# Optimization experiments

Measured on AMD Instinct MI355X. Metric: run time of the kernel, lower is better.

## Reference

```python
import jax, jax.numpy as jnp
import numpy as np

# QMon (monDEQ, Winston & Kolter): conv pre-net -> MONSingleConv + MONBorderReLU solved
# with Peaceman-Rachford splitting -> border crop -> MLP head.
BATCH = 256
C = 64            # DEQ channels
N = 9             # DEQ spatial dim (in_dim=9)
K = 3             # MONSingleConv kernel size
M_STRONG = 0.1    # m (strong monotonicity)
ALPHA = 1.0
TOL = 1e-5
MAX_ITER = 50
OUT_FEATURES = 18


def conv2d(x, w, b=None, stride=1):
    y = jax.lax.conv_general_dilated(x, w, (stride, stride), 'VALID',
                                     dimension_numbers=('NCHW', 'OIHW', 'NCHW'))
    if b is not None:
        y = y + b[None, :, None, None]
    return y


def circ_conv(x, w, b=None):
    # circular-padded 'same' conv (cpad + valid conv in the torch code)
    p = (w.shape[2] - 1) // 2
    xp = jnp.pad(x, ((0, 0), (0, 0), (p, p), (p, p)), mode='wrap')
    return conv2d(xp, w, b)


def circ_conv_T(x, w):
    # adjoint of circular conv = circular conv with spatially-flipped, channel-transposed kernel
    wt = jnp.transpose(jnp.flip(w, (2, 3)), (1, 0, 2, 3))
    return circ_conv(x, wt)


def W_multiply(z, A_w, g):
    # W z = (1-m) z - g * A^T A z, with A Frobenius-normalized
    An = A_w / jnp.linalg.norm(A_w)
    Az = circ_conv(z, An)
    ATAz = circ_conv_T(Az, An)
    return (1.0 - M_STRONG) * z - g * ATAz


def build_inverse(A_w, g, n):
    # ((1+alpha) I - alpha W)^{-1} per 2D-DFT frequency (circular conv is block-circulant)
    An = A_w / jnp.linalg.norm(A_w)
    co, ci, k, _ = An.shape
    p = (k - 1) // 2
    kimg = jnp.zeros((co, ci, n, n), An.dtype)
    for dx in range(k):
        for dy in range(k):
            kimg = kimg.at[:, :, (dx - p) % n, (dy - p) % n].set(An[:, :, dx, dy])
    Af = jnp.conj(jnp.fft.fft2(kimg)).transpose(2, 3, 0, 1)  # (n,n,O,I): A_hat(w)
    I = jnp.eye(co, dtype=Af.dtype)
    c = (1.0 + ALPHA) - ALPHA * (1.0 - M_STRONG)
    Mmat = c * I + (ALPHA * g).astype(Af.dtype) * jnp.einsum('xyoi,xyoj->xyij', jnp.conj(Af), Af)
    return jnp.linalg.inv(Mmat)  # (n,n,C,C) complex


def apply_inverse(Vinv, z):
    zf = jnp.fft.fft2(z)                                  # (B,C,n,n)
    yf = jnp.einsum('xyoc,bcxy->boxy', Vinv, zf)
    return jnp.real(jnp.fft.ifft2(yf)).astype(z.dtype)


def mon_deq(xpre, U_w, U_b, A_w, g):
    n = xpre.shape[-1]
    bias = circ_conv(xpre, U_w, U_b)
    Vinv = build_inverse(A_w, g, n)
    mask = jnp.pad(jnp.ones((n - 2, n - 2), xpre.dtype), 1)[None, None]  # MONBorderReLU border=1
    brelu = lambda v: jax.nn.relu(v) * mask
    z0 = jnp.zeros_like(bias)

    def body(state):
        z, u, err, it = state
        u12 = 2.0 * z - u
        z12 = apply_inverse(Vinv, u12 + ALPHA * bias)
        un = 2.0 * z12 - u12
        zn = brelu(un)
        err = jnp.linalg.norm(zn - z) / (1e-6 + jnp.linalg.norm(zn))
        return zn, un, err, it + 1

    def cond(state):
        _, _, err, it = state
        return (err > TOL) & (it < MAX_ITER)

    z, u, err, it = jax.lax.while_loop(cond, body, (z0, z0, jnp.asarray(1.0, xpre.dtype), 0))
    # final pass with the linear operator (as in the torch forward after the no_grad solve)
    return brelu(W_multiply(z, A_w, g) + bias)


def setup_inputs() -> dict:
    key = jax.random.key(0)
    ks = jax.random.split(key, 12)

    def u(k, shape, fan_in):
        b = 1.0 / np.sqrt(fan_in)
        return jax.random.uniform(k, shape, jnp.float32, -b, b)

    x = jax.random.uniform(ks[0], (BATCH, 4, 84, 84), jnp.float32) * 255.0
    return dict(
        x=x,
        conv1_w=u(ks[1], (32, 4, 8, 8), 4 * 8 * 8), conv1_b=u(ks[2], (32,), 4 * 8 * 8),
        conv2_w=u(ks[3], (64, 32, 4, 4), 32 * 4 * 4), conv2_b=u(ks[4], (64,), 32 * 4 * 4),
        U_w=u(ks[5], (C, C, K, K), C * K * K), U_b=u(ks[6], (C,), C * K * K),
        A_w=u(ks[7], (C, C, K, K), C * K * K), g=jnp.asarray(1.0, jnp.float32),
        fc1_w=u(ks[8], (512, 3136), 3136), fc1_b=u(ks[9], (512,), 3136),
        fc2_w=u(ks[10], (OUT_FEATURES, 512), 512), fc2_b=u(ks[11], (OUT_FEATURES,), 512),
    )


def reference(x, conv1_w, conv1_b, conv2_w, conv2_b, U_w, U_b, A_w, g,
              fc1_w, fc1_b, fc2_w, fc2_b):
    h = jax.nn.relu(conv2d(x / 255.0, conv1_w, conv1_b, stride=4))   # (B,32,20,20)
    h = jax.nn.relu(conv2d(h, conv2_w, conv2_b, stride=2))           # (B,64,9,9)
    z = mon_deq(h, U_w, U_b, A_w, g)                                 # (B,64,9,9)
    z = z[:, :, 1:-1, 1:-1].reshape(z.shape[0], -1)                  # (B,3136)
    h = jax.nn.relu(z @ fc1_w.T + fc1_b)
    return h @ fc2_w.T + fc2_b
```

## Files before the change

### kernel.cpp

```cpp
#include <hip/hip_runtime.h>


#define NB 256
#define NCH 64
#define NP 81
#define NIMG (NB*NCH)
#define MAXIT 50
#define NCAN 41
#define CANON(l) ((l) < 5 ? (l) : (l) + 4)

constexpr float C9[9] = {
  1.0f, 0.76604444311897803f, 0.17364817766693041f, -0.5f,
  -0.93969262078590843f, -0.93969262078590843f, -0.5f,
  0.17364817766693041f, 0.76604444311897803f };
constexpr float S9[9] = {
  0.0f, 0.64278760968653936f, 0.98480775301220802f, 0.86602540378443871f,
  0.34202014332566877f, -0.34202014332566877f, -0.86602540378443871f,
  -0.98480775301220802f, -0.64278760968653936f };

__constant__ float COS9[9] = {
  1.0f, 0.76604444311897803f, 0.17364817766693041f, -0.5f,
  -0.93969262078590843f, -0.93969262078590843f, -0.5f,
  0.17364817766693041f, 0.76604444311897803f };
__constant__ float SIN9[9] = {
  0.0f, 0.64278760968653936f, 0.98480775301220802f, 0.86602540378443871f,
  0.34202014332566877f, -0.34202014332566877f, -0.86602540378443871f,
  -0.98480775301220802f, -0.64278760968653936f };

__global__ __launch_bounds__(256) void k_norm(const float* __restrict__ Aw,
                                              float* __restrict__ sc) {
    __shared__ float red[256];
    float s = 0.f;
    for (int i = threadIdx.x; i < 64*64*9; i += 256) { float a = Aw[i]; s += a*a; }
    red[threadIdx.x] = s; __syncthreads();
    for (int w = 128; w > 0; w >>= 1) {
        if (threadIdx.x < w) red[threadIdx.x] += red[threadIdx.x + w];
        __syncthreads();
    }
    if (threadIdx.x == 0) { float n = sqrtf(red[0]); sc[0] = n; sc[1] = 1.f/n; }
}

__global__ __launch_bounds__(512, 4) void k_conv1(const float* __restrict__ x,
                                                  const float* __restrict__ w,
                                                  const float* __restrict__ bb,
                                                  float* __restrict__ y) {
    __shared__ float xl[2*7056];
    int blk = blockIdx.x, tid = threadIdx.x;
    int b = blk >> 1, og = (blk & 1) << 4;
    float acc[16];
    #pragma unroll
    for (int o = 0; o < 16; ++o) acc[o] = 0.f;
    int p = tid, oy = p/20, ox = p%20;
    for (int cp = 0; cp < 2; ++cp) {
        __syncthreads();
        const float4* xg = (const float4*)(x + b*28224 + cp*14112);
        for (int i = tid; i < 3528; i += 512) ((float4*)xl)[i] = xg[i];
        __syncthreads();
        if (p < 400) {
            #pragma unroll
            for (int ci = 0; ci < 2; ++ci)
            #pragma unroll
            for (int ky = 0; ky < 8; ++ky) {
                const float* xr = xl + ci*7056 + (oy*4+ky)*84 + ox*4;
                float4 x0 = *(const float4*)xr;
                float4 x1 = *(const float4*)(xr+4);
                const float* wr = w + og*256 + (cp*2+ci)*64 + ky*8;
                #pragma unroll
                for (int o = 0; o < 16; ++o) {
                    const float* wo = wr + o*256;
                    acc[o] += x0.x*wo[0] + x0.y*wo[1] + x0.z*wo[2] + x0.w*wo[3]
                            + x1.x*wo[4] + x1.y*wo[5] + x1.z*wo[6] + x1.w*wo[7];
                }
            }
        }
    }
    if (p < 400) {
        #pragma unroll
        for (int o = 0; o < 16; ++o)
            y[b*12800 + (og+o)*400 + p] = fmaxf(acc[o]*(1.f/255.f) + bb[og+o], 0.f);
    }
}

__global__ __launch_bounds__(512, 4) void k_conv2(const float* __restrict__ h1,
                                                  const float* __restrict__ w2,
                                                  const float* __restrict__ b2,
                                                  float* __restrict__ h2) {
    int blk = blockIdx.x, tid = threadIdx.x;
    int b = blk >> 1, og = (blk & 1) << 5;
    __shared__ float hl[12800];
    for (int i = tid; i < 12800; i += 512) {
        int ci = i / 400, pix = i % 400, iy = pix / 20, ix = pix % 20;
        hl[ci*400 + ((iy&1)*2 + (ix&1))*100 + (iy>>1)*10 + (ix>>1)] = h1[b*12800 + i];
    }
    __syncthreads();
    for (int idx = tid; idx < 2592; idx += 512) {
        int o = og + idx/81, p = idx%81, oy = p/9, ox = p%9;
        float acc = 0.f;
        const float* wo = w2 + o*512;
        for (int ci = 0; ci < 32; ci++) {
            const float* base = hl + ci*400;
            const float* wb = wo + ci*16;
            #pragma unroll
            for (int ky = 0; ky < 4; ky++)
            #pragma unroll
            for (int kx = 0; kx < 4; kx++)
                acc += base[((ky&1)*2 + (kx&1))*100 + (oy + (ky>>1))*10 + (ox + (kx>>1))]
                     * wb[ky*4 + kx];
        }
        h2[b*5184 + o*81 + p] = fmaxf(acc + b2[o], 0.f);
    }
}

__global__ __launch_bounds__(512, 4) void k_bias(const float* __restrict__ h2,
                                                 const float* __restrict__ Uw,
                                                 const float* __restrict__ Ub,
                                                 float* __restrict__ biasT) {
    int blk = blockIdx.x, tid = threadIdx.x;
    int b = blk >> 1, og = (blk & 1) << 5;
    __shared__ float h2l[5184];
    __shared__ float bt[2592];
    for (int i = tid; i < 5184; i += 512) h2l[i] = h2[b*5184 + i];
    __syncthreads();
    for (int idx = tid; idx < 2592; idx += 512) {
        int oc = idx/81, o = og + oc, p = idx%81, i0 = p/9, j0 = p%9;
        int im = (i0+8)%9, ip = (i0+1)%9, jm = (j0+8)%9, jp = (j0+1)%9;
        int r0 = im*9, r1 = i0*9, r2 = ip*9;
        float acc = 0.f;
        const float* wo = Uw + o*576;
        for (int ci = 0; ci < 64; ci++) {
            const float* hb = h2l + ci*81;
            const float* wb = wo + ci*9;
            acc += hb[r0+jm]*wb[0] + hb[r0+j0]*wb[1] + hb[r0+jp]*wb[2]
                 + hb[r1+jm]*wb[3] + hb[r1+j0]*wb[4] + hb[r1+jp]*wb[5]
                 + hb[r2+jm]*wb[6] + hb[r2+j0]*wb[7] + hb[r2+jp]*wb[8];
        }
        bt[oc*81 + p] = acc + Ub[o];
    }
    __syncthreads();
    for (int idx = tid; idx < 2592; idx += 512) {
        int p = idx >> 5, o32 = idx & 31;
        biasT[p*NIMG + b*64 + og + o32] = bt[o32*81 + p];
    }
}

__global__ __launch_bounds__(256) void k_af(const float* __restrict__ Aw,
                                            const float* __restrict__ sc,
                                            float2* __restrict__ Af) {
    int l = blockIdx.x; int f = CANON(l);
    int x = f/9, y = f%9;
    float inv = sc[1];
    for (int pr = threadIdx.x; pr < 4096; pr += 256) {
        const float* a = Aw + pr*9;
        float re = 0.f, im = 0.f;
        #pragma unroll
        for (int dx = 0; dx < 3; dx++)
        #pragma unroll
        for (int dy = 0; dy < 3; dy++) {
            int tt = (x*(dx+8) + y*(dy+8)) % 9;
            float v = a[dx*3+dy] * inv;
            re += v * COS9[tt]; im += v * SIN9[tt];
        }
        Af[f*4096 + pr] = make_float2(re, im);
    }
}

__global__ __launch_bounds__(256) void k_mw(const float2* __restrict__ Af,
                                            const float* __restrict__ gp,
                                            float2* __restrict__ Mmat,
                                            float2* __restrict__ WmT) {
    int l = blockIdx.x >> 2, q = blockIdx.x & 3;
    int f = CANON(l);
    float g = gp[0];
    __shared__ float2 Al[4096];
    for (int i = threadIdx.x; i < 4096; i += 256) Al[i] = Af[f*4096 + i];
    __syncthreads();
    int e = q*1024 + threadIdx.x;
    #pragma unroll
    for (int rep = 0; rep < 4; ++rep, e += 256) {
        int i = e >> 6, j = e & 63;
        float sr = 0.f, si = 0.f;
        for (int o = 0; o < 64; o++) {
            float2 a = Al[o*64 + i], b = Al[o*64 + j];
            sr += a.x*b.x + a.y*b.y;
            si += a.x*b.y - a.y*b.x;
        }
        Mmat[f*4096 + e] = make_float2((i==j ? 1.1f : 0.f) + g*sr, g*si);
        WmT [f*4096 + j*64 + i] = make_float2((i==j ? 0.9f : 0.f) - g*sr, -g*si);
    }
}

__global__ __launch_bounds__(256) void k_inv(float2* __restrict__ Mio) {
    int f = CANON((int)blockIdx.x);
    __shared__ float2 Mt[64*65];
    __shared__ float2 rowk[2][64];
    __shared__ float2 fcol[2][64];
    int tid = threadIdx.x;
    int i = tid & 63, jg = tid >> 6;
    float2* Mg = Mio + f*4096;
    for (int e = tid; e < 4096; e += 256) Mt[(e>>6)*65 + (e&63)] = Mg[e];
    __syncthreads();
    float2 r[16];
    #pragma unroll
    for (int jj = 0; jj < 16; ++jj) r[jj] = Mt[i*65 + jg*16 + jj];

    for (int k = 0; k < 64; ++k) {
        int buf = k & 1;
        if (i == k) {
            #pragma unroll
            for (int jj = 0; jj < 16; ++jj) rowk[buf][jg*16 + jj] = r[jj];
        }
        if (jg == (k >> 4)) {
            int sel = k & 15;
            float2 v = r[0];
            #pragma unroll
            for (int jj = 1; jj < 16; ++jj) v = (sel == jj) ? r[jj] : v;
            fcol[buf][i] = v;
        }
        __syncthreads();
        float2 d = rowk[buf][k];
        float den = 1.f / (d.x*d.x + d.y*d.y);
        float pr = d.x*den, pi = -d.y*den;
        float2 fi = fcol[buf][i];
        bool piv = (i == k);
        #pragma unroll
        for (int jj = 0; jj < 16; ++jj) {
            int j = jg*16 + jj;
            float2 rw = rowk[buf][j];
            float2 rkj = (j == k) ? make_float2(pr, pi)
                                  : make_float2(rw.x*pr - rw.y*pi,
                                                rw.x*pi + rw.y*pr);
            if (piv) {
                r[jj] = rkj;
            } else {
                float bx = (j == k) ? 0.f : r[jj].x;
                float by = (j == k) ? 0.f : r[jj].y;
                r[jj] = make_float2(bx - (fi.x*rkj.x - fi.y*rkj.y),
                                    by - (fi.x*rkj.y + fi.y*rkj.x));
            }
        }
    }
    __syncthreads();
    #pragma unroll
    for (int jj = 0; jj < 16; ++jj) Mt[(jg*16 + jj)*65 + i] = r[jj];
    __syncthreads();
    for (int e = tid; e < 4096; e += 256) Mg[e] = Mt[(e>>6)*65 + (e&63)];
}

__global__ __launch_bounds__(576) void k_fft(const float* __restrict__ biasT,
                                             float2* __restrict__ Tf) {
    __shared__ float2 T1[81*64];
    int lane = threadIdx.x & 63, j = threadIdx.x >> 6;
    int gimg = blockIdx.x*64 + lane;
    {
        int r = j;
        float tn[9];
        #pragma unroll
        for (int xc = 0; xc < 9; ++xc) tn[xc] = biasT[(r*9 + xc)*NIMG + gimg];
        #pragma unroll
        for (int ky = 0; ky < 9; ++ky) {
            float sr = 0.f, si = 0.f;
            #pragma unroll
            for (int xx = 0; xx < 9; ++xx) {
                const int m = (ky*xx) % 9;
                sr += tn[xx]*C9[m];
                si -= tn[xx]*S9[m];
            }
            T1[(r*9 + ky)*64 + lane] = make_float2(sr, si);
        }
    }
    __syncthreads();
    {
        int ky = j;
        float2 s[9];
        #pragma unroll
        for (int r = 0; r < 9; ++r) s[r] = T1[(r*9 + ky)*64 + lane];
        #pragma unroll
        for (int kx = 0; kx < 5; ++kx) {
            float fr = 0.f, fi = 0.f;
            #pragma unroll
            for (int r = 0; r < 9; ++r) {
                const int m = (kx*r) % 9;
                fr += s[r].x*C9[m] + s[r].y*S9[m];
                fi += s[r].y*C9[m] - s[r].x*S9[m];
            }
            if (kx > 0 || ky < 5)
                Tf[(kx*9 + ky)*NIMG + gimg] = make_float2(fr, fi);
        }
    }
}

__global__ __launch_bounds__(256) void k_mv(const float2* __restrict__ Tf,
                                            float2* __restrict__ Yf,
                                            const float2* __restrict__ V) {
    int l = blockIdx.x >> 4, bc = blockIdx.x & 15;
    int f = CANON(l);
    int lane = threadIdx.x & 63;
    int wid  = __builtin_amdgcn_readfirstlane((int)(threadIdx.x >> 6));
    int b0 = bc*16 + wid*4;
    const float2* Vg = V + f*4096 + lane;
    const float2* Tg = Tf + f*NIMG + b0*64;
    float2 a0 = make_float2(0.f,0.f), a1 = a0, a2 = a0, a3 = a0;
    #pragma unroll 8
    for (int c = 0; c < 64; ++c) {
        float2 v = Vg[c*64];
        float2 t0 = Tg[c], t1 = Tg[64+c], t2 = Tg[128+c], t3 = Tg[192+c];
        a0.x += v.x*t0.x - v.y*t0.y; a0.y += v.x*t0.y + v.y*t0.x;
        a1.x += v.x*t1.x - v.y*t1.y; a1.y += v.x*t1.y + v.y*t1.x;
        a2.x += v.x*t2.x - v.y*t2.y; a2.y += v.x*t2.y + v.y*t2.x;
        a3.x += v.x*t3.x - v.y*t3.y; a3.y += v.x*t3.y + v.y*t3.x;
    }
    float2* Yg = Yf + f*NIMG + b0*64 + lane;
    Yg[0] = a0; Yg[64] = a1; Yg[128] = a2; Yg[192] = a3;
}

__global__ __launch_bounds__(576) void k_fuse(const float2* __restrict__ Yf,
                                              float* __restrict__ u12T,
                                              const float* __restrict__ biasT,
                                              float2* __restrict__ Tf,
                                              int last) {
    __shared__ float2 T1[81*64];
    int lane = threadIdx.x & 63, j = threadIdx.x >> 6;
    int gimg = blockIdx.x*64 + lane;
    {
        int ky = j;
        float2 y[9];
        #pragma unroll
        for (int kx = 0; kx < 9; ++kx) {
            int fc; bool cj;
            if (kx == 0)      { cj = (ky >= 5); fc = cj ? (9 - ky) : ky; }
            else if (kx <= 4) { cj = false;     fc = kx*9 + ky; }
            else              { cj = true;      fc = (9-kx)*9 + (ky ? 9-ky : 0); }
            float2 a = Yf[fc*NIMG + gimg];
            y[kx] = make_float2(a.x, cj ? -a.y : a.y);
        }
        #pragma unroll
        for (int r = 0; r < 9; ++r) {
            float sr = 0.f, si = 0.f;
            #pragma unroll
            for (int kx = 0; kx < 9; ++kx) {
                const int m = (r*kx) % 9;
                sr += y[kx].x*C9[m] - y[kx].y*S9[m];
                si += y[kx].x*S9[m] + y[kx].y*C9[m];
            }
            T1[(r*9 + ky)*64 + lane] = make_float2(sr, si);
        }
    }
    __syncthreads();
    {
        int r = j;
        float2 t1[9];
        #pragma unroll
        for (int ky = 0; ky < 9; ++ky) t1[ky] = T1[(r*9 + ky)*64 + lane];
        float tn[9];
        #pragma unroll
        for (int xc = 0; xc < 9; ++xc) {
            float yr = 0.f;
            #pragma unroll
            for (int ky = 0; ky < 9; ++ky) {
                const int m = (xc*ky) % 9;
                yr += t1[ky].x*C9[m] - t1[ky].y*S9[m];
            }
            yr *= (1.f/81.f);
            int gi = (r*9 + xc)*NIMG + gimg;
            float u12v = u12T[gi];
            float un = 2.f*yr - u12v;
            bool interior = (r >= 1 && r <= 7 && xc >= 1 && xc <= 7);
            float zn = interior ? fmaxf(un, 0.f) : 0.f;
            float u12n = 2.f*zn - un;
            u12T[gi] = u12n;
            tn[xc] = last ? zn : (u12n + biasT[gi]);
        }
        #pragma unroll
        for (int ky = 0; ky < 9; ++ky) {
            float sr = 0.f, si = 0.f;
            #pragma unroll
            for (int xx = 0; xx < 9; ++xx) {
                const int m = (ky*xx) % 9;
                sr += tn[xx]*C9[m];
                si -= tn[xx]*S9[m];
            }
            T1[(r*9 + ky)*64 + lane] = make_float2(sr, si);
        }
    }
    __syncthreads();
    {
        int ky = j;
        float2 s[9];
        #pragma unroll
        for (int r = 0; r < 9; ++r) s[r] = T1[(r*9 + ky)*64 + lane];
        #pragma unroll
        for (int kx = 0; kx < 5; ++kx) {
            float fr = 0.f, fi = 0.f;
            #pragma unroll
            for (int r = 0; r < 9; ++r) {
                const int m = (kx*r) % 9;
                fr += s[r].x*C9[m] + s[r].y*S9[m];
                fi += s[r].y*C9[m] - s[r].x*S9[m];
            }
            if (kx > 0 || ky < 5)
                Tf[(kx*9 + ky)*NIMG + gimg] = make_float2(fr, fi);
        }
    }
}

__global__ __launch_bounds__(576) void k_crop(const float2* __restrict__ Yf,
                                              const float* __restrict__ biasT,
                                              float* __restrict__ zc) {
    __shared__ float2 T1[81*64];
    int lane = threadIdx.x & 63, j = threadIdx.x >> 6;
    int gimg = blockIdx.x*64 + lane;
    {
        int ky = j;
        float2 y[9];
        #pragma unroll
        for (int kx = 0; kx < 9; ++kx) {
            int fc; bool cj;
            if (kx == 0)      { cj = (ky >= 5); fc = cj ? (9 - ky) : ky; }
            else if (kx <= 4) { cj = false;     fc = kx*9 + ky; }
            else              { cj = true;      fc = (9-kx)*9 + (ky ? 9-ky : 0); }
            float2 a = Yf[fc*NIMG + gimg];
            y[kx] = make_float2(a.x, cj ? -a.y : a.y);
        }
        #pragma unroll
        for (int r = 0; r < 9; ++r) {
            float sr = 0.f, si = 0.f;
            #pragma unroll
            for (int kx = 0; kx < 9; ++kx) {
                const int m = (r*kx) % 9;
                sr += y[kx].x*C9[m] - y[kx].y*S9[m];
                si += y[kx].x*S9[m] + y[kx].y*C9[m];
            }
            T1[(r*9 + ky)*64 + lane] = make_float2(sr, si);
        }
    }
    __syncthreads();
    if (j >= 1 && j <= 7) {
        int r = j;
        float2 t1[9];
        #pragma unroll
        for (int ky = 0; ky < 9; ++ky) t1[ky] = T1[(r*9 + ky)*64 + lane];
        float* zr = zc + (gimg >> 6)*3136 + (gimg & 63)*49 + (r-1)*7;
        #pragma unroll
        for (int xc = 1; xc < 8; ++xc) {
            float yr = 0.f;
            #pragma unroll
            for (int ky = 0; ky < 9; ++ky) {
                const int m = (xc*ky) % 9;
                yr += t1[ky].x*C9[m] - t1[ky].y*S9[m];
            }
            yr *= (1.f/81.f);
            zr[xc-1] = fmaxf(yr + biasT[(r*9 + xc)*NIMG + gimg], 0.f);
        }
    }
}

__global__ __launch_bounds__(256) void k_fc1(const float* __restrict__ A,
                                             const float* __restrict__ W,
                                             const float* __restrict__ bb,
                                             float* __restrict__ H) {
    int bt = blockIdx.x >> 5, ot = blockIdx.x & 31;
    int b0 = bt*16, o0 = ot*16;
    __shared__ float At[16][65], Bt[16][65];
    int tid = threadIdx.x;
    int row = tid >> 6, col = tid & 63;
    int tb = tid >> 4, to = tid & 15;
    float acc = 0.f;
    for (int k0 = 0; k0 < 3136; k0 += 64) {
        #pragma unroll
        for (int s = 0; s < 4; s++) {
            int rr = row + s*4;
            At[rr][col] = A[(b0+rr)*3136 + k0 + col];
            Bt[rr][col] = W[(o0+rr)*3136 + k0 + col];
        }
        __syncthreads();
        #pragma unroll
        for (int kk = 0; kk < 64; kk++)
            acc += At[tb][kk] * Bt[to][kk];
        __syncthreads();
    }
    H[(b0+tb)*512 + o0+to] = fmaxf(acc + bb[o0+to], 0.f);
}

__global__ __launch_bounds__(256) void k_fc2(const float* __restrict__ H,
                                             const float* __restrict__ W,
                                             const float* __restrict__ bb,
                                             float* __restrict__ out) {
    int idx = blockIdx.x*256 + threadIdx.x;
    if (idx >= 4608) return;
    int b = idx/18, o = idx%18;
    const float* h = H + b*512;
    const float* w = W + o*512;
    float acc = 0.f;
    for (int k = 0; k < 512; k++) acc += h[k]*w[k];
    out[idx] = acc + bb[o];
}

extern "C" void kernel_launch(void* const* d_in, const int* in_sizes, int n_in,
                              void* d_out, int out_size, void* d_ws, size_t ws_size,
                              hipStream_t stream) {
    (void)in_sizes; (void)n_in; (void)out_size; (void)ws_size;
    const float* x   = (const float*)d_in[0];
    const float* c1w = (const float*)d_in[1];
    const float* c1b = (const float*)d_in[2];
    const float* c2w = (const float*)d_in[3];
    const float* c2b = (const float*)d_in[4];
    const float* Uw  = (const float*)d_in[5];
    const float* Ub  = (const float*)d_in[6];
    const float* Aw  = (const float*)d_in[7];
    const float* gp  = (const float*)d_in[8];
    const float* f1w = (const float*)d_in[9];
    const float* f1b = (const float*)d_in[10];
    const float* f2w = (const float*)d_in[11];
    const float* f2b = (const float*)d_in[12];

    float* ws = (float*)d_ws;
    float*  h1    = ws + 0;
    float2* Tf    = (float2*)(ws + 0);
    float*  biasT = ws + 3276800;
    float*  u12T  = ws + 4603904;
    float2* Yf    = (float2*)(ws + 5931008);
    float2* Af    = (float2*)(ws + 8585216);
    float2* Minv  = (float2*)(ws + 9248768);
    float2* WmT   = (float2*)(ws + 9912320);
    float*  zc    = ws + 10575872;
    float*  hfc   = ws + 11378688;
    float*  sc    = ws + 11509760;
    float*  h2    = ws + 11509764;

    hipMemsetAsync(u12T, 0, (size_t)1327104*sizeof(float), stream);

    k_norm <<<1,     256, 0, stream>>>(Aw, sc);
    k_conv1<<<512,   512, 0, stream>>>(x, c1w, c1b, h1);
    k_conv2<<<512,   512, 0, stream>>>(h1, c2w, c2b, h2);
    k_bias <<<512,   512, 0, stream>>>(h2, Uw, Ub, biasT);
    k_af   <<<NCAN,  256, 0, stream>>>(Aw, sc, Af);
    k_mw   <<<NCAN*4,256, 0, stream>>>(Af, gp, Minv, WmT);
    k_inv  <<<NCAN,  256, 0, stream>>>(Minv);

    k_fft<<<256, 576, 0, stream>>>(biasT, Tf);
    for (int it = 0; it < MAXIT; it++) {
        k_mv  <<<NCAN*16, 256, 0, stream>>>(Tf, Yf, Minv);
        k_fuse<<<256,     576, 0, stream>>>(Yf, u12T, biasT, Tf, it == MAXIT-1);
    }
    k_mv  <<<NCAN*16, 256, 0, stream>>>(Tf, Yf, WmT);
    k_crop<<<256,     576, 0, stream>>>(Yf, biasT, zc);

    k_fc1<<<512, 256, 0, stream>>>(zc, f1w, f1b, hfc);
    k_fc2<<<18,  256, 0, stream>>>(hfc, f2w, f2b, (float*)d_out);
}
```

Baseline: 1.860 ms.

## Exploit real-input Hermitian symmetry along y axis in per-iteration 2D DFTs

Changes the canonical half-spectrum from half-in-x to half-in-y, so the row DFT computes only 5 of 9 ky bins and the inverse row DFT uses the Hermitian doubling trick on 5 bins. This cuts the shared-memory intermediate from 81 to 45 entries per image and removes about 4/9 of the DFT work in the hot per-iteration kernels, though some warps now sit idle in the column phases. It also stages conv1 weights in shared memory with float4 reads in place of scalar global loads.

```diff
diff --git a/kernel.cpp b/kernel.cpp
--- a/kernel.cpp
+++ b/kernel.cpp
@@ -7,7 +7,9 @@
 #define NIMG (NB*NCH)
 #define MAXIT 50
 #define NCAN 41
-#define CANON(l) ((l) < 5 ? (l) : (l) + 4)
+__device__ __host__ inline int CAN2(int l) {
+    return (l < 5) ? l*9 : ((l-5)%9)*9 + ((l-5)/9 + 1);
+}
 
 constexpr float C9[9] = {
   1.0f, 0.76604444311897803f, 0.17364817766693041f, -0.5f,
@@ -45,8 +47,10 @@
                                                   const float* __restrict__ bb,
                                                   float* __restrict__ y) {
     __shared__ float xl[2*7056];
+    __shared__ float wl[16*256];
     int blk = blockIdx.x, tid = threadIdx.x;
     int b = blk >> 1, og = (blk & 1) << 4;
+    for (int i = tid; i < 4096; i += 512) wl[i] = w[og*256 + i];
     float acc[16];
     #pragma unroll
     for (int o = 0; o < 16; ++o) acc[o] = 0.f;
@@ -54,7 +58,7 @@
     for (int cp = 0; cp < 2; ++cp) {
         __syncthreads();
         const float4* xg = (const float4*)(x + b*28224 + cp*14112);
-        for (int i = tid; i < 3528; i += 512) ((float4*)xl)[i] = xg[i];
+        for (int i = tid; i < 3528; i += 512) ((float4*)(xl))[i] = xg[i];
         __syncthreads();
         if (p < 400) {
             #pragma unroll
@@ -64,12 +68,13 @@
                 const float* xr = xl + ci*7056 + (oy*4+ky)*84 + ox*4;
                 float4 x0 = *(const float4*)xr;
                 float4 x1 = *(const float4*)(xr+4);
-                const float* wr = w + og*256 + (cp*2+ci)*64 + ky*8;
+                const float* wr = wl + (cp*2+ci)*64 + ky*8;
                 #pragma unroll
                 for (int o = 0; o < 16; ++o) {
-                    const float* wo = wr + o*256;
-                    acc[o] += x0.x*wo[0] + x0.y*wo[1] + x0.z*wo[2] + x0.w*wo[3]
-                            + x1.x*wo[4] + x1.y*wo[5] + x1.z*wo[6] + x1.w*wo[7];
+                    float4 w0 = *(const float4*)(wr + o*256);
+                    float4 w1 = *(const float4*)(wr + o*256 + 4);
+                    acc[o] += x0.x*w0.x + x0.y*w0.y + x0.z*w0.z + x0.w*w0.w
+                            + x1.x*w1.x + x1.y*w1.y + x1.z*w1.z + x1.w*w1.w;
                 }
             }
         }
@@ -146,7 +151,7 @@
 __global__ __launch_bounds__(256) void k_af(const float* __restrict__ Aw,
                                             const float* __restrict__ sc,
                                             float2* __restrict__ Af) {
-    int l = blockIdx.x; int f = CANON(l);
+    int l = blockIdx.x; int f = CAN2(l);
     int x = f/9, y = f%9;
     float inv = sc[1];
     for (int pr = threadIdx.x; pr < 4096; pr += 256) {
@@ -169,7 +174,7 @@
                                             float2* __restrict__ Mmat,
                                             float2* __restrict__ WmT) {
     int l = blockIdx.x >> 2, q = blockIdx.x & 3;
-    int f = CANON(l);
+    int f = CAN2(l);
     float g = gp[0];
     __shared__ float2 Al[4096];
     for (int i = threadIdx.x; i < 4096; i += 256) Al[i] = Af[f*4096 + i];
@@ -190,7 +195,7 @@
 }
 
 __global__ __launch_bounds__(256) void k_inv(float2* __restrict__ Mio) {
-    int f = CANON((int)blockIdx.x);
+    int f = CAN2((int)blockIdx.x);
     __shared__ float2 Mt[64*65];
     __shared__ float2 rowk[2][64];
     __shared__ float2 fcol[2][64];
@@ -248,7 +253,7 @@
 
 __global__ __launch_bounds__(576) void k_fft(const float* __restrict__ biasT,
                                              float2* __restrict__ Tf) {
-    __shared__ float2 T1[81*64];
+    __shared__ float2 T1[9*5*64];
     int lane = threadIdx.x & 63, j = threadIdx.x >> 6;
     int gimg = blockIdx.x*64 + lane;
     {
@@ -257,7 +262,7 @@
         #pragma unroll
         for (int xc = 0; xc < 9; ++xc) tn[xc] = biasT[(r*9 + xc)*NIMG + gimg];
         #pragma unroll
-        for (int ky = 0; ky < 9; ++ky) {
+        for (int ky = 0; ky < 5; ++ky) {
             float sr = 0.f, si = 0.f;
             #pragma unroll
             for (int xx = 0; xx < 9; ++xx) {
@@ -265,26 +270,27 @@
                 sr += tn[xx]*C9[m];
                 si -= tn[xx]*S9[m];
             }
-            T1[(r*9 + ky)*64 + lane] = make_float2(sr, si);
-        }
-    }
-    __syncthreads();
-    {
+            T1[(r*5 + ky)*64 + lane] = make_float2(sr, si);
+        }
+    }
+    __syncthreads();
+    if (j < 5) {
         int ky = j;
         float2 s[9];
         #pragma unroll
-        for (int r = 0; r < 9; ++r) s[r] = T1[(r*9 + ky)*64 + lane];
-        #pragma unroll
-        for (int kx = 0; kx < 5; ++kx) {
-            float fr = 0.f, fi = 0.f;
-            #pragma unroll
-            for (int r = 0; r < 9; ++r) {
-                const int m = (kx*r) % 9;
-                fr += s[r].x*C9[m] + s[r].y*S9[m];
-                fi += s[r].y*C9[m] - s[r].x*S9[m];
-            }
-            if (kx > 0 || ky < 5)
+        for (int r = 0; r < 9; ++r) s[r] = T1[(r*5 + ky)*64 + lane];
+        #pragma unroll
+        for (int kx = 0; kx < 9; ++kx) {
+            if (kx < 5 || ky > 0) {
+                float fr = 0.f, fi = 0.f;
+                #pragma unroll
+                for (int r = 0; r < 9; ++r) {
+                    const int m = (kx*r) % 9;
+                    fr += s[r].x*C9[m] + s[r].y*S9[m];
+                    fi += s[r].y*C9[m] - s[r].x*S9[m];
+                }
                 Tf[(kx*9 + ky)*NIMG + gimg] = make_float2(fr, fi);
+            }
         }
     }
 }
@@ -293,7 +299,7 @@
                                             float2* __restrict__ Yf,
                                             const float2* __restrict__ V) {
     int l = blockIdx.x >> 4, bc = blockIdx.x & 15;
-    int f = CANON(l);
+    int f = CAN2(l);
     int lane = threadIdx.x & 63;
     int wid  = __builtin_amdgcn_readfirstlane((int)(threadIdx.x >> 6));
     int b0 = bc*16 + wid*4;
@@ -318,18 +324,17 @@
                                               const float* __restrict__ biasT,
                                               float2* __restrict__ Tf,
                                               int last) {
-    __shared__ float2 T1[81*64];
+    __shared__ float2 T1[9*5*64];
     int lane = threadIdx.x & 63, j = threadIdx.x >> 6;
     int gimg = blockIdx.x*64 + lane;
-    {
+    if (j < 5) {
         int ky = j;
         float2 y[9];
         #pragma unroll
         for (int kx = 0; kx < 9; ++kx) {
             int fc; bool cj;
-            if (kx == 0)      { cj = (ky >= 5); fc = cj ? (9 - ky) : ky; }
-            else if (kx <= 4) { cj = false;     fc = kx*9 + ky; }
-            else              { cj = true;      fc = (9-kx)*9 + (ky ? 9-ky : 0); }
+            if (ky == 0 && kx >= 5) { fc = (9 - kx)*9; cj = true; }
+            else                    { fc = kx*9 + ky;  cj = false; }
             float2 a = Yf[fc*NIMG + gimg];
             y[kx] = make_float2(a.x, cj ? -a.y : a.y);
         }
@@ -342,23 +347,23 @@
                 sr += y[kx].x*C9[m] - y[kx].y*S9[m];
                 si += y[kx].x*S9[m] + y[kx].y*C9[m];
             }
-            T1[(r*9 + ky)*64 + lane] = make_float2(sr, si);
+            T1[(r*5 + ky)*64 + lane] = make_float2(sr, si);
         }
     }
     __syncthreads();
     {
         int r = j;
-        float2 t1[9];
-        #pragma unroll
-        for (int ky = 0; ky < 9; ++ky) t1[ky] = T1[(r*9 + ky)*64 + lane];
+        float2 t1[5];
+        #pragma unroll
+        for (int ky = 0; ky < 5; ++ky) t1[ky] = T1[(r*5 + ky)*64 + lane];
         float tn[9];
         #pragma unroll
         for (int xc = 0; xc < 9; ++xc) {
-            float yr = 0.f;
-            #pragma unroll
-            for (int ky = 0; ky < 9; ++ky) {
+            float yr = t1[0].x;
+            #pragma unroll
+            for (int ky = 1; ky < 5; ++ky) {
                 const int m = (xc*ky) % 9;
-                yr += t1[ky].x*C9[m] - t1[ky].y*S9[m];
+                yr += 2.f*(t1[ky].x*C9[m] - t1[ky].y*S9[m]);
             }
             yr *= (1.f/81.f);
             int gi = (r*9 + xc)*NIMG + gimg;
@@ -371,7 +376,7 @@
             tn[xc] = last ? zn : (u12n + biasT[gi]);
         }
         #pragma unroll
-        for (int ky = 0; ky < 9; ++ky) {
+        for (int ky = 0; ky < 5; ++ky) {
             float sr = 0.f, si = 0.f;
             #pragma unroll
             for (int xx = 0; xx < 9; ++xx) {
@@ -379,26 +384,27 @@
                 sr += tn[xx]*C9[m];
                 si -= tn[xx]*S9[m];
             }
-            T1[(r*9 + ky)*64 + lane] = make_float2(sr, si);
-        }
-    }
-    __syncthreads();
-    {
+            T1[(r*5 + ky)*64 + lane] = make_float2(sr, si);
+        }
+    }
+    __syncthreads();
+    if (j < 5) {
         int ky = j;
         float2 s[9];
         #pragma unroll
-        for (int r = 0; r < 9; ++r) s[r] = T1[(r*9 + ky)*64 + lane];
-        #pragma unroll
-        for (int kx = 0; kx < 5; ++kx) {
-            float fr = 0.f, fi = 0.f;
-            #pragma unroll
-            for (int r = 0; r < 9; ++r) {
-                const int m = (kx*r) % 9;
-                fr += s[r].x*C9[m] + s[r].y*S9[m];
-                fi += s[r].y*C9[m] - s[r].x*S9[m];
-            }
-            if (kx > 0 || ky < 5)
+        for (int r = 0; r < 9; ++r) s[r] = T1[(r*5 + ky)*64 + lane];
+        #pragma unroll
+        for (int kx = 0; kx < 9; ++kx) {
+            if (kx < 5 || ky > 0) {
+                float fr = 0.f, fi = 0.f;
+                #pragma unroll
+                for (int r = 0; r < 9; ++r) {
+                    const int m = (kx*r) % 9;
+                    fr += s[r].x*C9[m] + s[r].y*S9[m];
+                    fi += s[r].y*C9[m] - s[r].x*S9[m];
+                }
                 Tf[(kx*9 + ky)*NIMG + gimg] = make_float2(fr, fi);
+            }
         }
     }
 }
@@ -406,18 +412,17 @@
 __global__ __launch_bounds__(576) void k_crop(const float2* __restrict__ Yf,
                                               const float* __restrict__ biasT,
                                               float* __restrict__ zc) {
-    __shared__ float2 T1[81*64];
+    __shared__ float2 T1[9*5*64];
     int lane = threadIdx.x & 63, j = threadIdx.x >> 6;
     int gimg = blockIdx.x*64 + lane;
-    {
+    if (j < 5) {
         int ky = j;
         float2 y[9];
         #pragma unroll
         for (int kx = 0; kx < 9; ++kx) {
             int fc; bool cj;
-            if (kx == 0)      { cj = (ky >= 5); fc = cj ? (9 - ky) : ky; }
-            else if (kx <= 4) { cj = false;     fc = kx*9 + ky; }
-            else              { cj = true;      fc = (9-kx)*9 + (ky ? 9-ky : 0); }
+            if (ky == 0 && kx >= 5) { fc = (9 - kx)*9; cj = true; }
+            else                    { fc = kx*9 + ky;  cj = false; }
             float2 a = Yf[fc*NIMG + gimg];
             y[kx] = make_float2(a.x, cj ? -a.y : a.y);
         }
@@ -430,23 +435,23 @@
                 sr += y[kx].x*C9[m] - y[kx].y*S9[m];
                 si += y[kx].x*S9[m] + y[kx].y*C9[m];
             }
-            T1[(r*9 + ky)*64 + lane] = make_float2(sr, si);
+            T1[(r*5 + ky)*64 + lane] = make_float2(sr, si);
         }
     }
     __syncthreads();
     if (j >= 1 && j <= 7) {
         int r = j;
-        float2 t1[9];
-        #pragma unroll
-        for (int ky = 0; ky < 9; ++ky) t1[ky] = T1[(r*9 + ky)*64 + lane];
+        float2 t1[5];
+        #pragma unroll
+        for (int ky = 0; ky < 5; ++ky) t1[ky] = T1[(r*5 + ky)*64 + lane];
         float* zr = zc + (gimg >> 6)*3136 + (gimg & 63)*49 + (r-1)*7;
         #pragma unroll
         for (int xc = 1; xc < 8; ++xc) {
-            float yr = 0.f;
-            #pragma unroll
-            for (int ky = 0; ky < 9; ++ky) {
+            float yr = t1[0].x;
+            #pragma unroll
+            for (int ky = 1; ky < 5; ++ky) {
                 const int m = (xc*ky) % 9;
-                yr += t1[ky].x*C9[m] - t1[ky].y*S9[m];
+                yr += 2.f*(t1[ky].x*C9[m] - t1[ky].y*S9[m]);
             }
             yr *= (1.f/81.f);
             zr[xc-1] = fmaxf(yr + biasT[(r*9 + xc)*NIMG + gimg], 0.f);
```

Result: slower. 2.090 ms (+12.4%).
